# Optimization experiments

Measured on AMD Instinct MI355X. Metric: run time of the kernel, lower is better.

Reference implementation:

```python
import jax, jax.numpy as jnp
import numpy as np

D_MODEL = 256
D_STATE = 1
HEADDIM = 32
NHEADS = D_MODEL // HEADDIM
HH = 64
WW = 64
BATCH = 2
L = HH * WW
D_IN_PROJ = (2 * D_MODEL + 2 * D_STATE + NHEADS) * 4


def _part1by1(n):
    n = n.astype(np.int64) & 0xFFFF
    n = (n | (n << 8)) & 0x00FF00FF
    n = (n | (n << 4)) & 0x0F0F0F0F
    n = (n | (n << 2)) & 0x33333333
    n = (n | (n << 1)) & 0x55555555
    return n


def _morton_indices(H, W):
    ys, xs = np.meshgrid(np.arange(H), np.arange(W), indexing='ij')
    ys, xs = ys.ravel(), xs.ravel()
    code_H = _part1by1(xs) | (_part1by1(ys) << 1)  # horizontal-first z-order
    code_V = _part1by1(ys) | (_part1by1(xs) << 1)  # vertical-first z-order
    mh = np.argsort(code_H, kind='stable').astype(np.int32)
    mv = np.argsort(code_V, kind='stable').astype(np.int32)
    ih = np.empty_like(mh); ih[mh] = np.arange(mh.size, dtype=np.int32)
    iv = np.empty_like(mv); iv[mv] = np.arange(mv.size, dtype=np.int32)
    return mh, mv, ih, iv


def setup_inputs() -> dict:
    key = jax.random.key(0)
    ks = jax.random.split(key, 12)
    x = jax.random.normal(ks[0], (BATCH, D_MODEL, HH, WW), dtype=jnp.float32)
    # RoPE tables: angles for L positions, HEADDIM/2 freqs
    freqs = 1.0 / (10000.0 ** (np.arange(0, HEADDIM, 2, dtype=np.float32) / HEADDIM))
    ang = np.outer(np.arange(L, dtype=np.float32), freqs)
    freqs_cos = jnp.asarray(np.cos(ang), dtype=jnp.float32)
    freqs_sin = jnp.asarray(np.sin(ang), dtype=jnp.float32)
    mh, mv, ih, iv = _morton_indices(HH, WW)
    # parameters
    W_in = jax.random.normal(ks[1], (D_MODEL, D_IN_PROJ), dtype=jnp.float32) * 0.02
    W_out = jax.random.normal(ks[2], (4 * D_MODEL, D_MODEL), dtype=jnp.float32) * 0.02
    conv_w = jax.random.normal(ks[3], (4, 2 * D_MODEL, 2 * D_MODEL, 3, 3), dtype=jnp.float32) * 0.02
    bn_gamma = jnp.ones((4, 2 * D_MODEL), dtype=jnp.float32)
    bn_beta = jnp.zeros((4, 2 * D_MODEL), dtype=jnp.float32)
    bn_mean = jax.random.normal(ks[4], (4, 2 * D_MODEL), dtype=jnp.float32) * 0.1
    bn_var = jax.random.uniform(ks[5], (4, 2 * D_MODEL), dtype=jnp.float32) * 0.5 + 0.5
    # dt bias init per module: inv softplus of dt ~ LogUniform(1e-3, 1e-1)
    u = np.asarray(jax.random.uniform(ks[6], (4, NHEADS)))
    dt = np.exp(u * (np.log(0.1) - np.log(0.001)) + np.log(0.001))
    dt_bias = jnp.asarray(dt + np.log(-np.expm1(-dt)), dtype=jnp.float32)
    A_log = jnp.log(jax.random.uniform(ks[7], (4, NHEADS), minval=1.0, maxval=16.0)).astype(jnp.float32)
    D = jnp.ones((4, NHEADS), dtype=jnp.float32)
    ln_gamma = jnp.ones((D_MODEL,), dtype=jnp.float32)
    ln_beta = jnp.zeros((D_MODEL,), dtype=jnp.float32)
    return dict(x=x, freqs_cos=freqs_cos, freqs_sin=freqs_sin,
                morton_H=jnp.asarray(mh), morton_V=jnp.asarray(mv),
                inv_H=jnp.asarray(ih), inv_V=jnp.asarray(iv),
                W_in=W_in, conv_w=conv_w, bn_gamma=bn_gamma, bn_beta=bn_beta,
                bn_mean=bn_mean, bn_var=bn_var, dt_bias=dt_bias, A_log=A_log,
                D=D, W_out=W_out, ln_gamma=ln_gamma, ln_beta=ln_beta)


def _rope(xh, cos, sin):
    # xh: [B,L,nh,hd]; complex multiply on (even,odd) pairs, matching view_as_complex
    xr, xi = xh[..., 0::2], xh[..., 1::2]
    c = cos[None, :, None, :]
    s = sin[None, :, None, :]
    out_r = xr * c - xi * s
    out_i = xr * s + xi * c
    return jnp.stack([out_r, out_i], axis=-1).reshape(xh.shape)


def _forward(x, freqs_cos, freqs_sin, morton_H, morton_V, inv_H, inv_V,
             W_in, conv_w, bn_gamma, bn_beta, bn_mean, bn_var,
             dt_bias, A_log, D, W_out, ln_gamma, ln_beta):
    B, C, H, W = x.shape
    Lh = H * W
    dim, ds, nh, hd = C, D_STATE, NHEADS, HEADDIM
    xf = x.reshape(B, C, Lh).transpose(0, 2, 1)            # [B,L,C]
    zxbcdt = xf @ W_in                                      # [B,L,d_in_proj]
    per = dim + (dim + 2 * ds) + nh
    specs = [(morton_H, inv_H, False), (morton_H, inv_H, True),
             (morton_V, inv_V, False), (morton_V, inv_V, True)]
    outs = []
    for d, (idx, iidx, flip) in enumerate(specs):
        blk = zxbcdt[..., d * per:(d + 1) * per]
        z = blk[..., :dim]
        xBC = blk[..., dim:2 * dim + 2 * ds]
        dt = blk[..., 2 * dim + 2 * ds:]
        xd, Bd, Cd = xBC[..., :dim], xBC[..., dim:dim + ds], xBC[..., dim + ds:]
        # depth-refine x,z with 3x3 conv + GELU + BN (eval)
        xz = jnp.concatenate([xd, z], axis=-1).transpose(0, 2, 1).reshape(B, 2 * C, H, W)
        xz = jax.lax.conv_general_dilated(xz, conv_w[d], (1, 1), 'SAME',
                                          dimension_numbers=('NCHW', 'OIHW', 'NCHW'))
        xz = jax.nn.gelu(xz)
        xz = (xz - bn_mean[d][None, :, None, None]) * jax.lax.rsqrt(bn_var[d] + 1e-3)[None, :, None, None] \
             * bn_gamma[d][None, :, None, None] + bn_beta[d][None, :, None, None]
        xz = xz.reshape(B, 2 * C, Lh).transpose(0, 2, 1)
        xd, zd = xz[..., :dim], xz[..., dim:]
        # morton reorder (+ flip for backward directions)
        def reord(a):
            a = jnp.take(a, idx, axis=1)
            return jnp.flip(a, axis=1) if flip else a
        xd, zd, Bd, Cd, dt = reord(xd), reord(zd), reord(Bd), reord(Cd), reord(dt)
        xh = _rope(xd.reshape(B, Lh, nh, hd), freqs_cos, freqs_sin)
        dtv = jax.nn.softplus(dt + dt_bias[d])              # [B,L,nh]
        A = -jnp.exp(A_log[d])                              # [nh]
        a = jnp.exp(dtv * A)                                # [B,L,nh]
        bterm = (dtv[..., None, None] * xh[..., None]) * Bd[:, :, None, None, :]  # [B,L,nh,hd,ds]
        def comb(c1, c2):
            a1, b1 = c1
            a2, b2 = c2
            return (a1 * a2, b1 * a2 + b2)
        _, h = jax.lax.associative_scan(comb, (a[..., None, None], bterm), axis=1)
        y = jnp.einsum('blhps,bls->blhp', h, Cd) + D[d][None, None, :, None] * xh
        y = y.reshape(B, Lh, dim) * (zd * jax.nn.sigmoid(zd))  # SiLU gate
        if flip:
            y = jnp.flip(y, axis=1)
        y = jnp.take(y, iidx, axis=1)                       # inverse morton
        outs.append(y)
    out = jnp.concatenate(outs, axis=-1) @ W_out            # [B,L,C]
    mu = out.mean(-1, keepdims=True)
    var = ((out - mu) ** 2).mean(-1, keepdims=True)
    out = (out - mu) * jax.lax.rsqrt(var + 1e-6) * ln_gamma + ln_beta
    return out.transpose(0, 2, 1).reshape(B, C, H, W)


def reference(x, freqs_cos, freqs_sin, morton_H, morton_V, inv_H, inv_V,
              W_in, conv_w, bn_gamma, bn_beta, bn_mean, bn_var,
              dt_bias, A_log, D, W_out, ln_gamma, ln_beta):
    return _forward(x, freqs_cos, freqs_sin, morton_H, morton_V, inv_H, inv_V,
                    W_in, conv_w, bn_gamma, bn_beta, bn_mean, bn_var,
                    dt_bias, A_log, D, W_out, ln_gamma, ln_beta)
```

## Files before the change

### kernel.cpp

```cpp
#include <hip/hip_runtime.h>
#include <math.h>

#define BATCH 2
#define CDIM 256
#define LLEN 4096
#define NH 8
#define HD 32
#define PER 522
#define NPROJ 2088
#define NPROJ_PAD 2112
#define NCHUNK 128
#define CLEN 32

typedef __attribute__((ext_vector_type(8))) short short8;
typedef __attribute__((ext_vector_type(4))) float f32x4;

static __device__ __forceinline__ ushort f2bf(float f) {
    unsigned u = __float_as_uint(f);
    u += 0x7fffu + ((u >> 16) & 1u);
    return (ushort)(u >> 16);
}
static __device__ __forceinline__ float bf2f(ushort u) {
    return __uint_as_float(((unsigned)u) << 16);
}

__global__ __launch_bounds__(256) void convert_wt(
    const float* __restrict__ W, ushort* __restrict__ Wt, int K, int N)
{
    __shared__ float tile[32][33];
    int n0 = blockIdx.x * 32, k0 = blockIdx.y * 32;
    int t = threadIdx.x;
    int nl = t & 31, kl = t >> 5;
    #pragma unroll
    for (int i = 0; i < 4; i++) {
        int n = n0 + nl;
        tile[kl + i * 8][nl] = (n < N) ? W[(long)(k0 + kl + i * 8) * N + n] : 0.f;
    }
    __syncthreads();
    int kl2 = t & 31, nl2 = t >> 5;
    #pragma unroll
    for (int i = 0; i < 4; i++)
        Wt[(long)(n0 + nl2 + i * 8) * K + k0 + kl2] = f2bf(tile[kl2][nl2 + i * 8]);
}

__global__ __launch_bounds__(256) void convert_x(
    const float* __restrict__ x, ushort* __restrict__ xbf)
{
    __shared__ float tile[32][33];
    int l0 = blockIdx.x * 32, c0 = blockIdx.y * 32, b = blockIdx.z;
    int t = threadIdx.x;
    int ll = t & 31, cl = t >> 5;
    #pragma unroll
    for (int i = 0; i < 4; i++)
        tile[cl + i * 8][ll] = x[((long)b * CDIM + c0 + cl + i * 8) * LLEN + l0 + ll];
    __syncthreads();
    int cl2 = t & 31, ll2 = t >> 5;
    #pragma unroll
    for (int i = 0; i < 4; i++)
        xbf[((long)b * LLEN + l0 + ll2 + i * 8) * CDIM + c0 + cl2] = f2bf(tile[cl2][ll2 + i * 8]);
}

__global__ __launch_bounds__(256) void convert_w(
    const float* __restrict__ cw, ushort* __restrict__ wbf)
{
    __shared__ ushort tmp[4608];
    int blk = blockIdx.x;
    int t = threadIdx.x;
    const float* src = cw + (long)blk * 4608;
    for (int q = t; q < 4608; q += 256) tmp[q] = f2bf(src[q]);
    __syncthreads();
    int d = blk >> 9, co = blk & 511;
    for (int q = t; q < 4608; q += 256) {
        int tt = q >> 9, ci = q & 511;
        wbf[(((long)(d * 9 + tt) * 512 + co) << 9) + ci] = tmp[ci * 9 + tt];
    }
}

__global__ __launch_bounds__(256) void gemm_in(
    const ushort* __restrict__ A, const ushort* __restrict__ Bt,
    ushort* __restrict__ cinb, float* __restrict__ bcdt)
{
    __shared__ ushort As[128][72];
    __shared__ ushort Bs[64][72];
    const int K = CDIM;
    int m0 = blockIdx.x * 128, n0 = blockIdx.y * 64;
    int t = threadIdx.x;
    int wave = t >> 6, lane = t & 63;
    int l15 = lane & 15, ko = lane >> 4;
    int mbase = wave * 32;

    f32x4 acc[2][4];
    #pragma unroll
    for (int mt = 0; mt < 2; mt++)
        #pragma unroll
        for (int nt = 0; nt < 4; nt++) acc[mt][nt] = (f32x4){0.f, 0.f, 0.f, 0.f};

    for (int k0 = 0; k0 < K; k0 += 64) {
        #pragma unroll
        for (int i = 0; i < 4; i++) {
            int g = t + 256 * i;
            int row = g >> 3, grp = g & 7;
            *(uint4*)&As[row][grp * 8] = *(const uint4*)&A[(long)(m0 + row) * K + k0 + grp * 8];
        }
        #pragma unroll
        for (int i = 0; i < 2; i++) {
            int g = t + 256 * i;
            int row = g >> 3, grp = g & 7;
            *(uint4*)&Bs[row][grp * 8] = *(const uint4*)&Bt[(long)(n0 + row) * K + k0 + grp * 8];
        }
        __syncthreads();
        #pragma unroll
        for (int kk = 0; kk < 2; kk++) {
            short8 a0 = *(const short8*)&As[mbase + l15][kk * 32 + ko * 8];
            short8 a1 = *(const short8*)&As[mbase + 16 + l15][kk * 32 + ko * 8];
            short8 bb[4];
            #pragma unroll
            for (int nt = 0; nt < 4; nt++)
                bb[nt] = *(const short8*)&Bs[nt * 16 + l15][kk * 32 + ko * 8];
            #pragma unroll
            for (int nt = 0; nt < 4; nt++) {
                acc[0][nt] = __builtin_amdgcn_mfma_f32_16x16x32_bf16(a0, bb[nt], acc[0][nt], 0, 0, 0);
                acc[1][nt] = __builtin_amdgcn_mfma_f32_16x16x32_bf16(a1, bb[nt], acc[1][nt], 0, 0, 0);
            }
        }
        __syncthreads();
    }
    #pragma unroll
    for (int nt = 0; nt < 4; nt++) {
        int n = n0 + nt * 16 + l15;
        if (n < NPROJ) {
            int d = n / PER;
            int r = n - d * PER;
            #pragma unroll
            for (int mt = 0; mt < 2; mt++)
                #pragma unroll
                for (int reg = 0; reg < 4; reg++) {
                    int m = m0 + mbase + mt * 16 + ko * 4 + reg;
                    int b = m >> 12, l = m & (LLEN - 1);
                    float v = acc[mt][nt][reg];
                    if (r < 512) {
                        int ch = (r < 256) ? (256 + r) : (r - 256);
                        cinb[(((long)d * BATCH + b) * LLEN + l) * 512 + ch] = f2bf(v);
                    } else {
                        bcdt[(long)m * 48 + d * 12 + (r - 512)] = v;
                    }
                }
        }
    }
}

__global__ __launch_bounds__(256) void gemm_bt(
    const ushort* __restrict__ A, const ushort* __restrict__ Bt, float* __restrict__ C,
    int K, int N)
{
    __shared__ ushort As[128][72];
    __shared__ ushort Bs[64][72];
    int m0 = blockIdx.x * 128, n0 = blockIdx.y * 64;
    int t = threadIdx.x;
    int wave = t >> 6, lane = t & 63;
    int l15 = lane & 15, ko = lane >> 4;
    int mbase = wave * 32;

    f32x4 acc[2][4];
    #pragma unroll
    for (int mt = 0; mt < 2; mt++)
        #pragma unroll
        for (int nt = 0; nt < 4; nt++) acc[mt][nt] = (f32x4){0.f, 0.f, 0.f, 0.f};

    for (int k0 = 0; k0 < K; k0 += 64) {
        #pragma unroll
        for (int i = 0; i < 4; i++) {
            int g = t + 256 * i;
            int row = g >> 3, grp = g & 7;
            *(uint4*)&As[row][grp * 8] = *(const uint4*)&A[(long)(m0 + row) * K + k0 + grp * 8];
        }
        #pragma unroll
        for (int i = 0; i < 2; i++) {
            int g = t + 256 * i;
            int row = g >> 3, grp = g & 7;
            *(uint4*)&Bs[row][grp * 8] = *(const uint4*)&Bt[(long)(n0 + row) * K + k0 + grp * 8];
        }
        __syncthreads();
        #pragma unroll
        for (int kk = 0; kk < 2; kk++) {
            short8 a0 = *(const short8*)&As[mbase + l15][kk * 32 + ko * 8];
            short8 a1 = *(const short8*)&As[mbase + 16 + l15][kk * 32 + ko * 8];
            short8 bb[4];
            #pragma unroll
            for (int nt = 0; nt < 4; nt++)
                bb[nt] = *(const short8*)&Bs[nt * 16 + l15][kk * 32 + ko * 8];
            #pragma unroll
            for (int nt = 0; nt < 4; nt++) {
                acc[0][nt] = __builtin_amdgcn_mfma_f32_16x16x32_bf16(a0, bb[nt], acc[0][nt], 0, 0, 0);
                acc[1][nt] = __builtin_amdgcn_mfma_f32_16x16x32_bf16(a1, bb[nt], acc[1][nt], 0, 0, 0);
            }
        }
        __syncthreads();
    }
    #pragma unroll
    for (int nt = 0; nt < 4; nt++) {
        int n = n0 + nt * 16 + l15;
        if (n < N) {
            #pragma unroll
            for (int mt = 0; mt < 2; mt++)
                #pragma unroll
                for (int reg = 0; reg < 4; reg++) {
                    int m = m0 + mbase + mt * 16 + ko * 4 + reg;
                    C[(long)m * N + n] = acc[mt][nt][reg];
                }
        }
    }
}

__global__ __launch_bounds__(256, 2) void conv_mfma(
    const ushort* __restrict__ cinb, const ushort* __restrict__ wbf,
    const float* __restrict__ bn_g, const float* __restrict__ bn_b,
    const float* __restrict__ bn_m, const float* __restrict__ bn_v,
    ushort* __restrict__ convb)
{
    __shared__ ushort in_s[6][4][66][8];

    int fid = blockIdx.x;
    int xcd = fid & 7;
    int k = fid >> 3;
    int slice = xcd * 4 + (k >> 5);
    int within = k & 31;
    int d = slice >> 3;
    int co0 = (slice & 7) * 64;
    int h0 = (within & 15) * 4;
    int b = within >> 4;
    int z = d * 2 + b;

    int t = threadIdx.x;
    int wave = t >> 6, lane = t & 63;
    int l15 = lane & 15, ko = lane >> 4;

    const ushort* conv_in = cinb + (long)z * LLEN * 512;
    ushort* conv_out = convb + (long)z * LLEN * 512;

    f32x4 acc[4][4];
    #pragma unroll
    for (int m = 0; m < 4; m++)
        #pragma unroll
        for (int nt = 0; nt < 4; nt++) acc[m][nt] = (f32x4){0.f, 0.f, 0.f, 0.f};

    const ushort* wtb = wbf + (long)d * 9 * 512 * 512 + (long)(co0 + l15) * 512 + ko * 8;

    for (int ci0 = 0; ci0 < 512; ci0 += 32) {
        for (int q = t; q < 1584; q += 256) {
            int oct = q & 3, pxg = q >> 2;
            int row = pxg / 66, px = pxg - row * 66;
            int hh = h0 + row - 1, wp = px - 1;
            uint4 val = make_uint4(0u, 0u, 0u, 0u);
            if (hh >= 0 && hh < 64 && wp >= 0 && wp < 64)
                val = *(const uint4*)&conv_in[(((long)hh) * 64 + wp) * 512 + ci0 + oct * 8];
            *(uint4*)&in_s[row][oct][px][0] = val;
        }
        const ushort* wp0 = wtb + ci0;
        short8 bw[4], bwn[4];
        #pragma unroll
        for (int nt = 0; nt < 4; nt++)
            bw[nt] = *(const short8*)&wp0[(long)nt * (16 * 512)];
        __syncthreads();
        #pragma unroll 1
        for (int tap = 0; tap < 9; tap++) {
            if (tap < 8) {
                const ushort* wq = wp0 + (long)(tap + 1) * (512 * 512);
                #pragma unroll
                for (int nt = 0; nt < 4; nt++)
                    bwn[nt] = *(const short8*)&wq[(long)nt * (16 * 512)];
            }
            int kh = (tap >= 6) ? 2 : ((tap >= 3) ? 1 : 0);
            int kw = tap - kh * 3;
            short8 av[4];
            #pragma unroll
            for (int m = 0; m < 4; m++)
                av[m] = *(const short8*)&in_s[wave + kh][ko][m * 16 + l15 + kw][0];
            #pragma unroll
            for (int m = 0; m < 4; m++)
                #pragma unroll
                for (int nt = 0; nt < 4; nt++)
                    acc[m][nt] = __builtin_amdgcn_mfma_f32_16x16x32_bf16(av[m], bw[nt], acc[m][nt], 0, 0, 0);
            #pragma unroll
            for (int nt = 0; nt < 4; nt++) bw[nt] = bwn[nt];
        }
        __syncthreads();
    }

    int hgl = h0 + wave;
    #pragma unroll
    for (int nt = 0; nt < 4; nt++) {
        int co = co0 + nt * 16 + l15;
        float mean = bn_m[d * 512 + co], var = bn_v[d * 512 + co];
        float g = bn_g[d * 512 + co], bbias = bn_b[d * 512 + co];
        float inv = rsqrtf(var + 1e-3f);
        #pragma unroll
        for (int m = 0; m < 4; m++)
            #pragma unroll
            for (int reg = 0; reg < 4; reg++) {
                int wc = m * 16 + ko * 4 + reg;
                float v = acc[m][nt][reg];
                float u = -1.5957691216057308f * (v + 0.044715f * v * v * v);
                v = v / (1.f + __expf(u));
                v = (v - mean) * inv * g + bbias;
                conv_out[((long)hgl * 64 + wc) * 512 + co] = f2bf(v);
            }
    }
}

__global__ __launch_bounds__(256) void scan_chunk(
    const float* __restrict__ bcdt, const ushort* __restrict__ conv_out,
    const int* __restrict__ mortonH, const int* __restrict__ mortonV,
    const float* __restrict__ fcos, const float* __restrict__ fsin,
    const float* __restrict__ dt_bias, const float* __restrict__ A_log,
    float* __restrict__ hfin, float* __restrict__ aprod_out)
{
    int chunk = blockIdx.x, b = blockIdx.y, d = blockIdx.z;
    const int* idx = (d < 2) ? mortonH : mortonV;
    int flip = d & 1;
    int c = threadIdx.x;
    int hh = c >> 5, p = c & 31;
    int i = p >> 1;
    float Acoef = -__expf(A_log[d * 8 + hh]);
    float dtb = dt_bias[d * 8 + hh];
    float hstate = 0.f, aprod = 1.f;
    const ushort* cop = conv_out + (long)(d * BATCH + b) * LLEN * 512;
    for (int jj = 0; jj < CLEN; jj++) {
        int j = chunk * CLEN + jj;
        int jsrc = flip ? (LLEN - 1 - j) : j;
        int src = idx[jsrc];
        const float* bc = bcdt + ((long)b * LLEN + src) * 48 + d * 12;
        float dtraw = bc[2 + hh] + dtb;
        float dtv = (dtraw > 20.f) ? dtraw : __logf(1.f + __expf(dtraw));
        float a = __expf(dtv * Acoef);
        float Bd = bc[0];
        const ushort* xrow = cop + (long)src * 512;
        uint xz = *(const uint*)&xrow[hh * 32 + (p & ~1)];
        float xe = bf2f((ushort)(xz & 0xffff));
        float xo = bf2f((ushort)(xz >> 16));
        float cs = fcos[j * 16 + i], sn = fsin[j * 16 + i];
        float xh = (p & 1) ? (xe * sn + xo * cs) : (xe * cs - xo * sn);
        hstate = a * hstate + dtv * xh * Bd;
        aprod *= a;
    }
    long o = (((long)(d * BATCH + b)) * NCHUNK + chunk) * 256 + c;
    hfin[o] = hstate;
    aprod_out[o] = aprod;
}

__global__ __launch_bounds__(256) void scan_final(
    const float* __restrict__ bcdt, const ushort* __restrict__ conv_out,
    const int* __restrict__ mortonH, const int* __restrict__ mortonV,
    const float* __restrict__ fcos, const float* __restrict__ fsin,
    const float* __restrict__ dt_bias, const float* __restrict__ A_log, const float* __restrict__ Dp,
    const float* __restrict__ hfin, const float* __restrict__ aprod, ushort* __restrict__ ycat)
{
    int chunk = blockIdx.x, b = blockIdx.y, d = blockIdx.z;
    const int* idx = (d < 2) ? mortonH : mortonV;
    int flip = d & 1;
    int c = threadIdx.x;
    int hh = c >> 5, p = c & 31;
    int i = p >> 1;
    float Acoef = -__expf(A_log[d * 8 + hh]);
    float dtb = dt_bias[d * 8 + hh];
    float Dv = Dp[d * 8 + hh];
    float hstate = 0.f;
    {
        long ob = ((long)(d * BATCH + b)) * NCHUNK;
        for (int ch = 0; ch < chunk; ch++) {
            long o = (ob + ch) * 256 + c;
            hstate = aprod[o] * hstate + hfin[o];
        }
    }
    const ushort* cop = conv_out + (long)(d * BATCH + b) * LLEN * 512;
    for (int jj = 0; jj < CLEN; jj++) {
        int j = chunk * CLEN + jj;
        int jsrc = flip ? (LLEN - 1 - j) : j;
        int src = idx[jsrc];
        const float* bc = bcdt + ((long)b * LLEN + src) * 48 + d * 12;
        float dtraw = bc[2 + hh] + dtb;
        float dtv = (dtraw > 20.f) ? dtraw : __logf(1.f + __expf(dtraw));
        float a = __expf(dtv * Acoef);
        float Bd = bc[0];
        float Cd = bc[1];
        const ushort* xrow = cop + (long)src * 512;
        uint xz = *(const uint*)&xrow[hh * 32 + (p & ~1)];
        float xe = bf2f((ushort)(xz & 0xffff));
        float xo = bf2f((ushort)(xz >> 16));
        float cs = fcos[j * 16 + i], sn = fsin[j * 16 + i];
        float xh = (p & 1) ? (xe * sn + xo * cs) : (xe * cs - xo * sn);
        hstate = a * hstate + dtv * xh * Bd;
        float y = hstate * Cd + Dv * xh;
        float zd = bf2f(xrow[256 + c]);
        y *= zd / (1.f + __expf(-zd));
        ycat[((long)b * LLEN + src) * 1024 + d * 256 + c] = f2bf(y);
    }
}

__global__ __launch_bounds__(256) void ln_out(
    const float* __restrict__ pre, const float* __restrict__ g, const float* __restrict__ bta,
    float* __restrict__ out)
{
    int row = blockIdx.x;
    int c = threadIdx.x;
    float v = pre[(long)row * 256 + c];
    float s = v, s2 = v * v;
    #pragma unroll
    for (int o = 32; o > 0; o >>= 1) {
        s += __shfl_down(s, o);
        s2 += __shfl_down(s2, o);
    }
    __shared__ float ss[4], ss2[4];
    __shared__ float mean_s, inv_s;
    int wid = c >> 6;
    if ((c & 63) == 0) { ss[wid] = s; ss2[wid] = s2; }
    __syncthreads();
    if (c == 0) {
        float S = ss[0] + ss[1] + ss[2] + ss[3];
        float S2 = ss2[0] + ss2[1] + ss2[2] + ss2[3];
        float mean = S / 256.f;
        float var = S2 / 256.f - mean * mean;
        mean_s = mean;
        inv_s = rsqrtf(var + 1e-6f);
    }
    __syncthreads();
    float o = (v - mean_s) * inv_s * g[c] + bta[c];
    int b = row >> 12, l = row & (LLEN - 1);
    out[((long)b * 256 + c) * (long)LLEN + l] = o;
}

extern "C" void kernel_launch(void* const* d_in, const int* in_sizes, int n_in,
                              void* d_out, int out_size, void* d_ws, size_t ws_size,
                              hipStream_t stream)
{
    const float* x        = (const float*)d_in[0];
    const float* fcos     = (const float*)d_in[1];
    const float* fsin     = (const float*)d_in[2];
    const int*   mortonH  = (const int*)d_in[3];
    const int*   mortonV  = (const int*)d_in[4];
    const float* W_in     = (const float*)d_in[7];
    const float* conv_w   = (const float*)d_in[8];
    const float* bn_g     = (const float*)d_in[9];
    const float* bn_b     = (const float*)d_in[10];
    const float* bn_m     = (const float*)d_in[11];
    const float* bn_v     = (const float*)d_in[12];
    const float* dt_bias  = (const float*)d_in[13];
    const float* A_log    = (const float*)d_in[14];
    const float* Dp       = (const float*)d_in[15];
    const float* W_out    = (const float*)d_in[16];
    const float* ln_g     = (const float*)d_in[17];
    const float* ln_b     = (const float*)d_in[18];
    float* out = (float*)d_out;

    float* ws = (float*)d_ws;
    const long CONVB_OFF   = 0;
    const long HFIN_OFF    = CONVB_OFF + 8388608;
    const long APROD_OFF   = HFIN_OFF + 4L * BATCH * NCHUNK * 256;
    const long BCDT_OFF    = APROD_OFF + 4L * BATCH * NCHUNK * 256;
    const long WBF_OFF     = BCDT_OFF + (long)BATCH * LLEN * 48;
    const long CINB_OFF    = WBF_OFF + 4718592;
    const long XBF_OFF     = CINB_OFF + 8388608;
    const long WINT_OFF    = XBF_OFF + 1048576;
    const long WOUTT_OFF   = WINT_OFF + 270336;
    const long YCATB_OFF   = WOUTT_OFF + 131072;
    const long PRE_OFF     = YCATB_OFF + 4194304;

    ushort* convb   = (ushort*)(ws + CONVB_OFF);
    float* hfin     = ws + HFIN_OFF;
    float* aprod    = ws + APROD_OFF;
    float* bcdt     = ws + BCDT_OFF;
    ushort* wbf     = (ushort*)(ws + WBF_OFF);
    ushort* cinb    = (ushort*)(ws + CINB_OFF);
    ushort* xbf     = (ushort*)(ws + XBF_OFF);
    ushort* wint    = (ushort*)(ws + WINT_OFF);
    ushort* woutt   = (ushort*)(ws + WOUTT_OFF);
    ushort* ycatb   = (ushort*)(ws + YCATB_OFF);
    float* pre      = ws + PRE_OFF;

    convert_w<<<4 * 512, 256, 0, stream>>>(conv_w, wbf);
    convert_wt<<<dim3(NPROJ_PAD / 32, CDIM / 32), 256, 0, stream>>>(W_in, wint, CDIM, NPROJ);
    convert_wt<<<dim3(CDIM / 32, 1024 / 32), 256, 0, stream>>>(W_out, woutt, 1024, CDIM);
    convert_x<<<dim3(LLEN / 32, CDIM / 32, BATCH), 256, 0, stream>>>(x, xbf);

    gemm_in<<<dim3(64, NPROJ_PAD / 64), 256, 0, stream>>>(xbf, wint, cinb, bcdt);

    conv_mfma<<<1024, 256, 0, stream>>>(
        cinb, wbf, bn_g, bn_b, bn_m, bn_v, convb);

    scan_chunk<<<dim3(NCHUNK, BATCH, 4), 256, 0, stream>>>(
        bcdt, convb, mortonH, mortonV, fcos, fsin, dt_bias, A_log, hfin, aprod);
    scan_final<<<dim3(NCHUNK, BATCH, 4), 256, 0, stream>>>(
        bcdt, convb, mortonH, mortonV, fcos, fsin, dt_bias, A_log, Dp, hfin, aprod, ycatb);

    gemm_bt<<<dim3(64, CDIM / 64), 256, 0, stream>>>(ycatb, woutt, pre, 1024, CDIM);

    ln_out<<<BATCH * LLEN, 256, 0, stream>>>(pre, ln_g, ln_b, out);
}
```

Baseline: 420.0 us.

## Halve scan chunk length and make LayerNorm one-wave-per-row

Chunk count for the chunked scan doubles (chunk length 16), giving more parallel blocks and shorter sequential loops per chunk, at the cost of a longer cross-chunk carry pass. The output LayerNorm now assigns one 64-lane wave per row using float4 loads and wave shuffles only, removing shared-memory reductions and block barriers. Its transposed stores stay strided, now four per lane.

```diff
diff --git a/kernel.cpp b/kernel.cpp
--- a/kernel.cpp
+++ b/kernel.cpp
@@ -9,8 +9,8 @@
 #define PER 522
 #define NPROJ 2088
 #define NPROJ_PAD 2112
-#define NCHUNK 128
-#define CLEN 32
+#define NCHUNK 256
+#define CLEN 16
 
 typedef __attribute__((ext_vector_type(8))) short short8;
 typedef __attribute__((ext_vector_type(4))) float f32x4;
@@ -401,32 +401,28 @@
     const float* __restrict__ pre, const float* __restrict__ g, const float* __restrict__ bta,
     float* __restrict__ out)
 {
-    int row = blockIdx.x;
-    int c = threadIdx.x;
-    float v = pre[(long)row * 256 + c];
-    float s = v, s2 = v * v;
+    int wave = threadIdx.x >> 6, lane = threadIdx.x & 63;
+    int row = blockIdx.x * 4 + wave;
+    float4 v = *(const float4*)&pre[(long)row * 256 + lane * 4];
+    float s = v.x + v.y + v.z + v.w;
+    float s2 = v.x * v.x + v.y * v.y + v.z * v.z + v.w * v.w;
     #pragma unroll
     for (int o = 32; o > 0; o >>= 1) {
         s += __shfl_down(s, o);
         s2 += __shfl_down(s2, o);
     }
-    __shared__ float ss[4], ss2[4];
-    __shared__ float mean_s, inv_s;
-    int wid = c >> 6;
-    if ((c & 63) == 0) { ss[wid] = s; ss2[wid] = s2; }
-    __syncthreads();
-    if (c == 0) {
-        float S = ss[0] + ss[1] + ss[2] + ss[3];
-        float S2 = ss2[0] + ss2[1] + ss2[2] + ss2[3];
-        float mean = S / 256.f;
-        float var = S2 / 256.f - mean * mean;
-        mean_s = mean;
-        inv_s = rsqrtf(var + 1e-6f);
-    }
-    __syncthreads();
-    float o = (v - mean_s) * inv_s * g[c] + bta[c];
+    s = __shfl(s, 0);
+    s2 = __shfl(s2, 0);
+    float mean = s * (1.f / 256.f);
+    float inv = rsqrtf(s2 * (1.f / 256.f) - mean * mean + 1e-6f);
+    float4 gg = *(const float4*)&g[lane * 4];
+    float4 bb = *(const float4*)&bta[lane * 4];
     int b = row >> 12, l = row & (LLEN - 1);
-    out[((long)b * 256 + c) * (long)LLEN + l] = o;
+    float* ob = out + ((long)b * 256 + lane * 4) * (long)LLEN + l;
+    ob[0]            = (v.x - mean) * inv * gg.x + bb.x;
+    ob[LLEN]         = (v.y - mean) * inv * gg.y + bb.y;
+    ob[2 * LLEN]     = (v.z - mean) * inv * gg.z + bb.z;
+    ob[3 * LLEN]     = (v.w - mean) * inv * gg.w + bb.w;
 }
 
 extern "C" void kernel_launch(void* const* d_in, const int* in_sizes, int n_in,
@@ -494,5 +490,5 @@
 
     gemm_bt<<<dim3(64, CDIM / 64), 256, 0, stream>>>(ycatb, woutt, pre, 1024, CDIM);
 
-    ln_out<<<BATCH * LLEN, 256, 0, stream>>>(pre, ln_g, ln_b, out);
-}
+    ln_out<<<BATCH * LLEN / 4, 256, 0, stream>>>(pre, ln_g, ln_b, out);
+}
```

Result: slower. 459.0 us (+9.3%).
